# Kernel tuning notes

Measured on AMD Instinct MI355X. Metric: run time of the kernel, lower is better.

## Reference

```python
import jax, jax.numpy as jnp
import numpy as np

L = 5          # num_layers
N = 50000      # nodes
E = 600000     # edges
D = 128        # num_features == hidden_units
G = 256        # graphs in batch
O = 10         # num_outputs
BN_EPS = 1e-5


def setup_inputs() -> dict:
    key = jax.random.key(0)
    ks = jax.random.split(key, 8)
    x = jax.random.normal(ks[0], (N, D), jnp.float32)
    edge_index = jax.random.randint(ks[1], (2, E), 0, N, jnp.int32)
    edge_attr = jax.random.randint(ks[2], (E, 3), 0, 8, jnp.int32)
    batch = jnp.sort(jax.random.randint(ks[3], (N,), 0, G, jnp.int32))
    s = 0.05
    return {
        "x": x,
        "edge_index": edge_index,
        "edge_attr": edge_attr,
        "batch": batch,
        "bond_emb": jax.random.normal(ks[4], (L, 3, 8, D), jnp.float32) * s,
        "conv_w1": jax.random.normal(ks[5], (L, D, D), jnp.float32) * s,
        "conv_b1": jnp.zeros((L, D), jnp.float32),
        "conv_bn_gamma": jnp.ones((L, D), jnp.float32),
        "conv_bn_beta": jnp.zeros((L, D), jnp.float32),
        "conv_bn_mean": jnp.zeros((L, D), jnp.float32),
        "conv_bn_var": jnp.ones((L, D), jnp.float32),
        "conv_w2": jax.random.normal(ks[6], (L, D, D), jnp.float32) * s,
        "conv_b2": jnp.zeros((L, D), jnp.float32),
        "bn_gamma": jnp.ones((L, D), jnp.float32),
        "bn_beta": jnp.zeros((L, D), jnp.float32),
        "bn_mean": jnp.zeros((L, D), jnp.float32),
        "bn_var": jnp.ones((L, D), jnp.float32),
        "fc_w": jax.random.normal(ks[7], (L + 1, D, O), jnp.float32) * s,
        "fc_b": jnp.zeros((L + 1, O), jnp.float32),
    }


def _bn_eval(h, gamma, beta, mean, var):
    return (h - mean) * jax.lax.rsqrt(var + BN_EPS) * gamma + beta


def reference(x, edge_index, edge_attr, batch, bond_emb,
              conv_w1, conv_b1, conv_bn_gamma, conv_bn_beta, conv_bn_mean, conv_bn_var,
              conv_w2, conv_b2, bn_gamma, bn_beta, bn_mean, bn_var, fc_w, fc_b):
    src, dst = edge_index[0], edge_index[1]  # x_j = x[src], aggregate at dst
    feat_ids = jnp.arange(3)
    outs = [x]
    for i in range(L):
        # BondEncoder: sum of per-feature embeddings -> [E, D]
        ea = bond_emb[i][feat_ids, edge_attr].sum(axis=1)
        # GINEConv (eps=0): msg = relu(x_j + edge_attr), scatter-add, nn(x + aggr)
        msg = jax.nn.relu(x[src] + ea)
        aggr = jax.ops.segment_sum(msg, dst, num_segments=N)
        h = x + aggr
        h = h @ conv_w1[i] + conv_b1[i]
        h = jax.nn.relu(_bn_eval(h, conv_bn_gamma[i], conv_bn_beta[i], conv_bn_mean[i], conv_bn_var[i]))
        h = h @ conv_w2[i] + conv_b2[i]
        x = jax.nn.relu(_bn_eval(h, bn_gamma[i], bn_beta[i], bn_mean[i], bn_var[i]))
        outs.append(x)
    # global mean pool per layer output, linear head, sum (dropout = identity in eval)
    counts = jax.ops.segment_sum(jnp.ones((N,), x.dtype), batch, num_segments=G)
    inv = 1.0 / jnp.maximum(counts, 1.0)
    out = jnp.zeros((G, O), x.dtype)
    for i, h in enumerate(outs):
        pooled = jax.ops.segment_sum(h, batch, num_segments=G) * inv[:, None]
        out = out + pooled @ fc_w[i] + fc_b[i]
    return out
```

## Files before the change

kernel.cpp:

```cpp
#include <hip/hip_runtime.h>

#define NN 50000
#define EE 600000
#define DD 128
#define GG 256
#define LL 5
#define OO 10
#define BN_EPS 1e-5f
#define CPAD 515
#define ESTRIDE 40

#define B_SCAT  2344
#define B_COMBO 1288
#define B_WT    160
#define B_CVT   3125
#define B_POOL  2048
#define B_PREP  (B_SCAT + B_COMBO + B_WT + B_CVT + B_POOL)

typedef __attribute__((ext_vector_type(8))) short short8;
typedef __attribute__((ext_vector_type(16))) float float16;

__device__ __forceinline__ unsigned short f2b(float f) {
    unsigned u = __float_as_uint(f);
    unsigned r = u + 0x7FFFu + ((u >> 16) & 1u);
    return (unsigned short)(r >> 16);
}
__device__ __forceinline__ unsigned pk2(float lo, float hi) {
    return (unsigned)f2b(lo) | ((unsigned)f2b(hi) << 16);
}
__device__ __forceinline__ float blo(unsigned u) { return __uint_as_float(u << 16); }
__device__ __forceinline__ float bhi(unsigned u) { return __uint_as_float(u & 0xFFFF0000u); }

__device__ __forceinline__ void acc8(float* acc, uint4 xv, uint4 cv) {
    acc[0] += fmaxf(blo(xv.x) + blo(cv.x), 0.f);
    acc[1] += fmaxf(bhi(xv.x) + bhi(cv.x), 0.f);
    acc[2] += fmaxf(blo(xv.y) + blo(cv.y), 0.f);
    acc[3] += fmaxf(bhi(xv.y) + bhi(cv.y), 0.f);
    acc[4] += fmaxf(blo(xv.z) + blo(cv.z), 0.f);
    acc[5] += fmaxf(bhi(xv.z) + bhi(cv.z), 0.f);
    acc[6] += fmaxf(blo(xv.w) + blo(cv.w), 0.f);
    acc[7] += fmaxf(bhi(xv.w) + bhi(cv.w), 0.f);
}

__launch_bounds__(256)
__global__ void prep(const float* __restrict__ x, const int* __restrict__ ei,
                     const int* __restrict__ eattr, const int* __restrict__ batch,
                     const float* __restrict__ bond,
                     const float* __restrict__ w1, const float* __restrict__ w2,
                     unsigned* __restrict__ xb4, unsigned short* __restrict__ combo,
                     short* __restrict__ wt, int* __restrict__ epos,
                     unsigned* __restrict__ e_info, float* __restrict__ pooled0) {
    const int bid = (int)(((long long)blockIdx.x * 1021) % B_PREP);
    const int t = threadIdx.x;
    if (bid < B_SCAT) {
        int e = bid * 256 + t;
        if (e < EE) {
            int dst = ei[EE + e];
            int slot = atomicAdd(&epos[dst], 1);
            if (slot < ESTRIDE) {
                unsigned cidx = (unsigned)eattr[e * 3 + 0] | ((unsigned)eattr[e * 3 + 1] << 3)
                              | ((unsigned)eattr[e * 3 + 2] << 6);
                e_info[dst * ESTRIDE + slot] = (unsigned)ei[e] | (cidx << 16);
            }
        }
    } else if (bid < B_SCAT + B_COMBO) {
        int e = (bid - B_SCAT) * 256 + t;
        if (e < LL * CPAD * DD) {
            int l = e / (CPAD * DD), rem = e - l * (CPAD * DD);
            int c = rem / DD, d = rem - c * DD;
            float s;
            if (c >= 512) s = -1e30f;
            else {
                const float* b_ = bond + (size_t)l * 3 * 8 * DD;
                s = b_[(c & 7) * DD + d] + b_[(8 + ((c >> 3) & 7)) * DD + d]
                  + b_[(16 + (c >> 6)) * DD + d];
            }
            combo[e] = f2b(s);
        }
    } else if (bid < B_SCAT + B_COMBO + B_WT) {
        __shared__ float tile[32][33];
        int b = bid - B_SCAT - B_COMBO;
        int mat = b >> 4, tl = b & 15;
        int k0 = (tl >> 2) * 32, c0 = (tl & 3) * 32;
        const float* W = (mat < 5) ? (w1 + (size_t)mat * DD * DD)
                                   : (w2 + (size_t)(mat - 5) * DD * DD);
        int j = t & 31, q = t >> 5;
#pragma unroll
        for (int rr = 0; rr < 4; ++rr) {
            int row = q + rr * 8;
            tile[row][j] = W[(size_t)(k0 + row) * DD + c0 + j];
        }
        __syncthreads();
#pragma unroll
        for (int rr = 0; rr < 4; ++rr) {
            int cr = q + rr * 8;
            wt[(size_t)mat * DD * DD + (size_t)(c0 + cr) * DD + k0 + j] = (short)f2b(tile[j][cr]);
        }
    } else if (bid < B_SCAT + B_COMBO + B_WT + B_CVT) {
        int gid = (bid - (B_SCAT + B_COMBO + B_WT)) * 256 + t;
        const float4* xp = (const float4*)(x + (size_t)gid * 8);
        float4 a = xp[0], c4 = xp[1];
        uint4 o;
        o.x = pk2(a.x, a.y); o.y = pk2(a.z, a.w);
        o.z = pk2(c4.x, c4.y); o.w = pk2(c4.z, c4.w);
        ((uint4*)xb4)[gid] = o;
    } else {
        __shared__ float sm[DD];
        int b = bid - (B_SCAT + B_COMBO + B_WT + B_CVT);
        int g = b >> 3, s = b & 7;
        int r0, r1;
        {
            int lo = 0, hi = NN;
            while (lo < hi) { int m = (lo + hi) >> 1; if (batch[m] < g) lo = m + 1; else hi = m; }
            r0 = lo;
            lo = 0; hi = NN;
            while (lo < hi) { int m = (lo + hi) >> 1; if (batch[m] < g + 1) lo = m + 1; else hi = m; }
            r1 = lo;
        }
        int col = t & 127, par = t >> 7;
        float ssum = 0.f;
        for (int r = r0 + s * 2 + par; r < r1; r += 16) ssum += x[(size_t)r * DD + col];
        if (par == 0) sm[col] = ssum;
        __syncthreads();
        if (par == 1) {
            float v = sm[col] + ssum;
            if (v != 0.f) atomicAdd(&pooled0[(size_t)g * DD + col], v);
        }
    }
}

__launch_bounds__(256)
__global__ void aggr_csr(const unsigned short* __restrict__ xin,
                         const int* __restrict__ epos,
                         const unsigned* __restrict__ e_info,
                         const unsigned short* __restrict__ combo,
                         unsigned short* __restrict__ hin) {
    const int q = 12500 / 8, rr_ = 12500 % 8;
    int xcd = blockIdx.x & 7, idx = blockIdx.x >> 3;
    int bid = (xcd < rr_ ? xcd * (q + 1) : rr_ * (q + 1) + (xcd - rr_) * q) + idx;
    int node = bid * 4 + (threadIdx.x >> 6);
    int lane = threadIdx.x & 63;
    if (node >= NN) return;
    const int base = node * ESTRIDE;
    int deg = epos[node]; if (deg > ESTRIDE) deg = ESTRIDE;
    const int eg = lane >> 4;
    const int f  = (lane & 15) * 8;

    unsigned i0 = __builtin_nontemporal_load(e_info + base + eg);
    unsigned i1 = __builtin_nontemporal_load(e_info + base + 4 + eg);
    unsigned i2 = __builtin_nontemporal_load(e_info + base + 8 + eg);
    unsigned i3 = __builtin_nontemporal_load(e_info + base + 12 + eg);

    uint4 xv0 = *(const uint4*)&xin[(size_t)(i0 & 0xFFFFu) * DD + f];
    uint4 cv0 = *(const uint4*)&combo[(size_t)(i0 >> 16) * DD + f];
    uint4 xv1 = *(const uint4*)&xin[(size_t)(i1 & 0xFFFFu) * DD + f];
    uint4 cv1 = *(const uint4*)&combo[(size_t)(i1 >> 16) * DD + f];
    uint4 xv2 = *(const uint4*)&xin[(size_t)(i2 & 0xFFFFu) * DD + f];
    uint4 cv2 = *(const uint4*)&combo[(size_t)(i2 >> 16) * DD + f];
    uint4 xv3 = *(const uint4*)&xin[(size_t)(i3 & 0xFFFFu) * DD + f];
    uint4 cv3 = *(const uint4*)&combo[(size_t)(i3 >> 16) * DD + f];

    float acc[8];
#pragma unroll
    for (int i = 0; i < 8; ++i) acc[i] = 0.f;
    acc8(acc, xv0, cv0);
    acc8(acc, xv1, cv1);
    acc8(acc, xv2, cv2);
    acc8(acc, xv3, cv3);

    if (deg > 16) {
        const int pe = base + ((deg + 7) & ~7);
        for (int p = base + 16; p < pe; p += 8) {
            unsigned j0 = __builtin_nontemporal_load(e_info + p + eg);
            unsigned j1 = __builtin_nontemporal_load(e_info + p + 4 + eg);
            uint4 ax0 = *(const uint4*)&xin[(size_t)(j0 & 0xFFFFu) * DD + f];
            uint4 ac0 = *(const uint4*)&combo[(size_t)(j0 >> 16) * DD + f];
            uint4 ax1 = *(const uint4*)&xin[(size_t)(j1 & 0xFFFFu) * DD + f];
            uint4 ac1 = *(const uint4*)&combo[(size_t)(j1 >> 16) * DD + f];
            acc8(acc, ax0, ac0);
            acc8(acc, ax1, ac1);
        }
    }

#pragma unroll
    for (int i = 0; i < 8; ++i) {
        acc[i] += __shfl_xor(acc[i], 16, 64);
        acc[i] += __shfl_xor(acc[i], 32, 64);
    }
    if (lane < 16) {
        uint4 self = *(const uint4*)&xin[(size_t)node * DD + f];
        uint4 o;
        o.x = pk2(acc[0] + blo(self.x), acc[1] + bhi(self.x));
        o.y = pk2(acc[2] + blo(self.y), acc[3] + bhi(self.y));
        o.z = pk2(acc[4] + blo(self.z), acc[5] + bhi(self.z));
        o.w = pk2(acc[6] + blo(self.w), acc[7] + bhi(self.w));
        *(uint4*)&hin[(size_t)node * DD + f] = o;
    }
}

__launch_bounds__(256)
__global__ void conv_fused(const unsigned short* __restrict__ hin,
                           const short* __restrict__ Wt1, const short* __restrict__ Wt2,
                           const float* __restrict__ b1, const float* __restrict__ g1,
                           const float* __restrict__ be1, const float* __restrict__ m1,
                           const float* __restrict__ v1,
                           const float* __restrict__ b2, const float* __restrict__ g2,
                           const float* __restrict__ be2, const float* __restrict__ m2,
                           const float* __restrict__ v2,
                           const int* __restrict__ batch,
                           unsigned short* __restrict__ outb,
                           float* __restrict__ pool_slot) {
    __shared__ short As[32 * 136];
    __shared__ int sbg[32];
    const int tid  = threadIdx.x;
    const int lane = tid & 63;
    const int wave = tid >> 6;
    const int row0 = blockIdx.x * 32;

    const int col   = wave * 32 + (lane & 31);
    const int khalf = (lane >> 5) * 8;
    const int arow  = lane & 31;
    const int rbase = 4 * (lane >> 5);
    const int gmin  = batch[row0];

    short8 bf[8];
#pragma unroll
    for (int ch = 0; ch < 8; ++ch)
        bf[ch] = *(const short8*)&Wt1[col * DD + ch * 16 + khalf];

    const float sc1 = g1[col] * rsqrtf(v1[col] + BN_EPS);
    const float sh1 = fmaf(b1[col] - m1[col], sc1, be1[col]);
    const float sc2 = g2[col] * rsqrtf(v2[col] + BN_EPS);
    const float sh2 = fmaf(b2[col] - m2[col], sc2, be2[col]);

    if (tid < 32) {
        int row = row0 + tid;
        sbg[tid] = (row < NN) ? batch[row] - gmin : -1;
    }
    for (int i = tid; i < 512; i += 256) {
        int r = i >> 4, c8 = (i & 15) * 8;
        int row = row0 + r;
        uint4 z = make_uint4(0, 0, 0, 0);
        if (row < NN) z = *(const uint4*)&hin[(size_t)row * DD + c8];
        *(uint4*)&As[r * 136 + c8] = z;
    }
    __syncthreads();

    float16 acc0 = {0.f,0.f,0.f,0.f,0.f,0.f,0.f,0.f,0.f,0.f,0.f,0.f,0.f,0.f,0.f,0.f};
#pragma unroll
    for (int ch = 0; ch < 8; ++ch) {
        short8 a0 = *(const short8*)&As[arow * 136 + ch * 16 + khalf];
        acc0 = __builtin_amdgcn_mfma_f32_32x32x16_bf16(a0, bf[ch], acc0, 0, 0, 0);
    }

#pragma unroll
    for (int ch = 0; ch < 8; ++ch)
        bf[ch] = *(const short8*)&Wt2[col * DD + ch * 16 + khalf];

    __syncthreads();
#pragma unroll
    for (int r = 0; r < 16; ++r) {
        int rl = (r & 3) + 8 * (r >> 2) + rbase;
        As[rl * 136 + col] = (short)f2b(fmaxf(fmaf(acc0[r], sc1, sh1), 0.f));
    }
    __syncthreads();

    acc0 = float16{0.f,0.f,0.f,0.f,0.f,0.f,0.f,0.f,0.f,0.f,0.f,0.f,0.f,0.f,0.f,0.f};
#pragma unroll
    for (int ch = 0; ch < 8; ++ch) {
        short8 a0 = *(const short8*)&As[arow * 136 + ch * 16 + khalf];
        acc0 = __builtin_amdgcn_mfma_f32_32x32x16_bf16(a0, bf[ch], acc0, 0, 0, 0);
    }

    float pg0 = 0.f, pg1 = 0.f, pg2 = 0.f, pg3 = 0.f;
#pragma unroll
    for (int r = 0; r < 16; ++r) {
        int rl  = (r & 3) + 8 * (r >> 2) + rbase;
        int row = row0 + rl;
        float v0 = fmaxf(fmaf(acc0[r], sc2, sh2), 0.f);
        if (row < NN) outb[(size_t)row * DD + col] = f2b(v0);
        int ga = sbg[rl];
        pg0 += (ga == 0) ? v0 : 0.f;
        pg1 += (ga == 1) ? v0 : 0.f;
        pg2 += (ga == 2) ? v0 : 0.f;
        pg3 += (ga == 3) ? v0 : 0.f;
    }
    pg0 += __shfl_down(pg0, 32);
    pg1 += __shfl_down(pg1, 32);
    pg2 += __shfl_down(pg2, 32);
    pg3 += __shfl_down(pg3, 32);
    if (lane < 32) {
        if (pg0 != 0.f)                  atomicAdd(&pool_slot[(gmin    ) * DD + col], pg0);
        if (pg1 != 0.f && gmin + 1 < GG) atomicAdd(&pool_slot[(gmin + 1) * DD + col], pg1);
        if (pg2 != 0.f && gmin + 2 < GG) atomicAdd(&pool_slot[(gmin + 2) * DD + col], pg2);
        if (pg3 != 0.f && gmin + 3 < GG) atomicAdd(&pool_slot[(gmin + 3) * DD + col], pg3);
    }
}

__launch_bounds__(64)
__global__ void head(const int* __restrict__ batch, const float* __restrict__ pooled,
                     const float* __restrict__ fcw, const float* __restrict__ fcb,
                     float* __restrict__ out) {
    int g = blockIdx.x, t = threadIdx.x;
    __shared__ float part[LL + 1][OO];
    int r0, r1;
    {
        int lo = 0, hi = NN;
        while (lo < hi) { int m = (lo + hi) >> 1; if (batch[m] < g) lo = m + 1; else hi = m; }
        r0 = lo;
        lo = 0; hi = NN;
        while (lo < hi) { int m = (lo + hi) >> 1; if (batch[m] < g + 1) lo = m + 1; else hi = m; }
        r1 = lo;
    }
    const float invg = 1.0f / fmaxf((float)(r1 - r0), 1.0f);
    if (t < (LL + 1) * OO) {
        int l = t / OO, o2 = t - l * OO;
        const float* p = pooled + ((size_t)l * GG + g) * DD;
        const float* w = fcw + (size_t)l * DD * OO + o2;
        float s = 0.f;
        for (int d2 = 0; d2 < DD; ++d2) s = fmaf(p[d2], w[(size_t)d2 * OO], s);
        part[l][o2] = s;
    }
    __syncthreads();
    if (t < OO) {
        float sp = 0.f, sb2 = 0.f;
#pragma unroll
        for (int l = 0; l < LL + 1; ++l) { sp += part[l][t]; sb2 += fcb[l * OO + t]; }
        out[g * OO + t] = sp * invg + sb2;
    }
}

extern "C" void kernel_launch(void* const* d_in, const int* in_sizes, int n_in,
                              void* d_out, int out_size, void* d_ws, size_t ws_size,
                              hipStream_t stream) {
    const float* x_in    = (const float*)d_in[0];
    const int*   ei      = (const int*)d_in[1];
    const int*   eattr   = (const int*)d_in[2];
    const int*   batch   = (const int*)d_in[3];
    const float* bond    = (const float*)d_in[4];
    const float* conv_w1 = (const float*)d_in[5];
    const float* conv_b1 = (const float*)d_in[6];
    const float* cbg     = (const float*)d_in[7];
    const float* cbb     = (const float*)d_in[8];
    const float* cbm     = (const float*)d_in[9];
    const float* cbv     = (const float*)d_in[10];
    const float* conv_w2 = (const float*)d_in[11];
    const float* conv_b2 = (const float*)d_in[12];
    const float* bg      = (const float*)d_in[13];
    const float* bb      = (const float*)d_in[14];
    const float* bm      = (const float*)d_in[15];
    const float* bv      = (const float*)d_in[16];
    const float* fcw     = (const float*)d_in[17];
    const float* fcb     = (const float*)d_in[18];
    float* out = (float*)d_out;

    char* base = (char*)d_ws;
    size_t o = 0;
    auto carve = [&](size_t bytes) { void* p = base + o; o += (bytes + 15) & ~(size_t)15; return p; };
    unsigned short* xbA    = (unsigned short*)carve((size_t)NN * DD * 2);
    unsigned short* xbB    = (unsigned short*)carve((size_t)NN * DD * 2);
    unsigned short* combo  = (unsigned short*)carve((size_t)LL * CPAD * DD * 2);
    short*          wt     = (short*)carve((size_t)10 * DD * DD * 2);
    const size_t ZBYTES = (size_t)NN * 4 + (size_t)(LL + 1) * GG * DD * 4;
    int*            epos   = (int*)carve(ZBYTES);
    float*          pooled = (float*)((char*)epos + (size_t)NN * 4);
    unsigned*       e_info = (unsigned*)carve((size_t)NN * ESTRIDE * 4);

    hipMemsetAsync(epos, 0, ZBYTES, stream);
    hipMemsetAsync(e_info, 0x02, (size_t)NN * ESTRIDE * 4, stream);

    prep<<<B_PREP, 256, 0, stream>>>(x_in, ei, eattr, batch, bond, conv_w1, conv_w2,
                                     (unsigned*)xbA, combo, wt, epos, e_info, pooled);

    const int conv_blocks = (NN + 31) / 32;
    const int aggr_blocks = (NN + 3) / 4;
    unsigned short* xin  = xbA;
    unsigned short* xout = xbB;
    for (int i = 0; i < LL; ++i) {
        aggr_csr<<<aggr_blocks, 256, 0, stream>>>(
            xin, epos, e_info, combo + (size_t)i * CPAD * DD, xout);
        conv_fused<<<conv_blocks, 256, 0, stream>>>(
            xout, wt + (size_t)i * DD * DD, wt + (size_t)(5 + i) * DD * DD,
            conv_b1 + (size_t)i * DD, cbg + (size_t)i * DD, cbb + (size_t)i * DD,
            cbm + (size_t)i * DD, cbv + (size_t)i * DD,
            conv_b2 + (size_t)i * DD, bg + (size_t)i * DD, bb + (size_t)i * DD,
            bm + (size_t)i * DD, bv + (size_t)i * DD,
            batch, xin, pooled + (size_t)(i + 1) * GG * DD);
    }
    head<<<GG, 64, 0, stream>>>(batch, pooled, fcw, fcb, out);
}
```

Measured before the change: 423.6 us.

## Fuse edge aggregation into per-layer MLP kernel via shared-memory staging

```diff
diff --git a/kernel.cpp b/kernel.cpp
--- a/kernel.cpp
+++ b/kernel.cpp
@@ -130,98 +130,102 @@
 }
 
 __launch_bounds__(256)
-__global__ void aggr_csr(const unsigned short* __restrict__ xin,
-                         const int* __restrict__ epos,
-                         const unsigned* __restrict__ e_info,
-                         const unsigned short* __restrict__ combo,
-                         unsigned short* __restrict__ hin) {
-    const int q = 12500 / 8, rr_ = 12500 % 8;
-    int xcd = blockIdx.x & 7, idx = blockIdx.x >> 3;
-    int bid = (xcd < rr_ ? xcd * (q + 1) : rr_ * (q + 1) + (xcd - rr_) * q) + idx;
-    int node = bid * 4 + (threadIdx.x >> 6);
-    int lane = threadIdx.x & 63;
-    if (node >= NN) return;
-    const int base = node * ESTRIDE;
-    int deg = epos[node]; if (deg > ESTRIDE) deg = ESTRIDE;
-    const int eg = lane >> 4;
-    const int f  = (lane & 15) * 8;
-
-    unsigned i0 = __builtin_nontemporal_load(e_info + base + eg);
-    unsigned i1 = __builtin_nontemporal_load(e_info + base + 4 + eg);
-    unsigned i2 = __builtin_nontemporal_load(e_info + base + 8 + eg);
-    unsigned i3 = __builtin_nontemporal_load(e_info + base + 12 + eg);
-
-    uint4 xv0 = *(const uint4*)&xin[(size_t)(i0 & 0xFFFFu) * DD + f];
-    uint4 cv0 = *(const uint4*)&combo[(size_t)(i0 >> 16) * DD + f];
-    uint4 xv1 = *(const uint4*)&xin[(size_t)(i1 & 0xFFFFu) * DD + f];
-    uint4 cv1 = *(const uint4*)&combo[(size_t)(i1 >> 16) * DD + f];
-    uint4 xv2 = *(const uint4*)&xin[(size_t)(i2 & 0xFFFFu) * DD + f];
-    uint4 cv2 = *(const uint4*)&combo[(size_t)(i2 >> 16) * DD + f];
-    uint4 xv3 = *(const uint4*)&xin[(size_t)(i3 & 0xFFFFu) * DD + f];
-    uint4 cv3 = *(const uint4*)&combo[(size_t)(i3 >> 16) * DD + f];
-
-    float acc[8];
-#pragma unroll
-    for (int i = 0; i < 8; ++i) acc[i] = 0.f;
-    acc8(acc, xv0, cv0);
-    acc8(acc, xv1, cv1);
-    acc8(acc, xv2, cv2);
-    acc8(acc, xv3, cv3);
-
-    if (deg > 16) {
-        const int pe = base + ((deg + 7) & ~7);
-        for (int p = base + 16; p < pe; p += 8) {
-            unsigned j0 = __builtin_nontemporal_load(e_info + p + eg);
-            unsigned j1 = __builtin_nontemporal_load(e_info + p + 4 + eg);
-            uint4 ax0 = *(const uint4*)&xin[(size_t)(j0 & 0xFFFFu) * DD + f];
-            uint4 ac0 = *(const uint4*)&combo[(size_t)(j0 >> 16) * DD + f];
-            uint4 ax1 = *(const uint4*)&xin[(size_t)(j1 & 0xFFFFu) * DD + f];
-            uint4 ac1 = *(const uint4*)&combo[(size_t)(j1 >> 16) * DD + f];
-            acc8(acc, ax0, ac0);
-            acc8(acc, ax1, ac1);
-        }
-    }
-
-#pragma unroll
-    for (int i = 0; i < 8; ++i) {
-        acc[i] += __shfl_xor(acc[i], 16, 64);
-        acc[i] += __shfl_xor(acc[i], 32, 64);
-    }
-    if (lane < 16) {
-        uint4 self = *(const uint4*)&xin[(size_t)node * DD + f];
-        uint4 o;
-        o.x = pk2(acc[0] + blo(self.x), acc[1] + bhi(self.x));
-        o.y = pk2(acc[2] + blo(self.y), acc[3] + bhi(self.y));
-        o.z = pk2(acc[4] + blo(self.z), acc[5] + bhi(self.z));
-        o.w = pk2(acc[6] + blo(self.w), acc[7] + bhi(self.w));
-        *(uint4*)&hin[(size_t)node * DD + f] = o;
-    }
-}
-
-__launch_bounds__(256)
-__global__ void conv_fused(const unsigned short* __restrict__ hin,
-                           const short* __restrict__ Wt1, const short* __restrict__ Wt2,
-                           const float* __restrict__ b1, const float* __restrict__ g1,
-                           const float* __restrict__ be1, const float* __restrict__ m1,
-                           const float* __restrict__ v1,
-                           const float* __restrict__ b2, const float* __restrict__ g2,
-                           const float* __restrict__ be2, const float* __restrict__ m2,
-                           const float* __restrict__ v2,
-                           const int* __restrict__ batch,
-                           unsigned short* __restrict__ outb,
-                           float* __restrict__ pool_slot) {
+__global__ void layer_fused(const unsigned short* __restrict__ xin,
+                            const int* __restrict__ epos,
+                            const unsigned* __restrict__ e_info,
+                            const unsigned short* __restrict__ combo,
+                            const short* __restrict__ Wt1, const short* __restrict__ Wt2,
+                            const float* __restrict__ b1, const float* __restrict__ g1,
+                            const float* __restrict__ be1, const float* __restrict__ m1,
+                            const float* __restrict__ v1,
+                            const float* __restrict__ b2, const float* __restrict__ g2,
+                            const float* __restrict__ be2, const float* __restrict__ m2,
+                            const float* __restrict__ v2,
+                            const int* __restrict__ batch,
+                            unsigned short* __restrict__ xout,
+                            float* __restrict__ pool_slot) {
     __shared__ short As[32 * 136];
     __shared__ int sbg[32];
     const int tid  = threadIdx.x;
     const int lane = tid & 63;
     const int wave = tid >> 6;
     const int row0 = blockIdx.x * 32;
+    const int gmin = batch[row0];
+
+    if (tid < 32) {
+        int row = row0 + tid;
+        sbg[tid] = (row < NN) ? batch[row] - gmin : -1;
+    }
+
+    const int eg = lane >> 4;
+    const int f  = (lane & 15) * 8;
+    for (int k = 0; k < 8; ++k) {
+        const int nl = wave * 8 + k;
+        const int node = row0 + nl;
+        if (node < NN) {
+            const int base = node * ESTRIDE;
+            unsigned i0 = __builtin_nontemporal_load(e_info + base + eg);
+            unsigned i1 = __builtin_nontemporal_load(e_info + base + 4 + eg);
+            unsigned i2 = __builtin_nontemporal_load(e_info + base + 8 + eg);
+            unsigned i3 = __builtin_nontemporal_load(e_info + base + 12 + eg);
+
+            uint4 xv0 = *(const uint4*)&xin[(size_t)(i0 & 0xFFFFu) * DD + f];
+            uint4 cv0 = *(const uint4*)&combo[(size_t)(i0 >> 16) * DD + f];
+            uint4 xv1 = *(const uint4*)&xin[(size_t)(i1 & 0xFFFFu) * DD + f];
+            uint4 cv1 = *(const uint4*)&combo[(size_t)(i1 >> 16) * DD + f];
+            uint4 xv2 = *(const uint4*)&xin[(size_t)(i2 & 0xFFFFu) * DD + f];
+            uint4 cv2 = *(const uint4*)&combo[(size_t)(i2 >> 16) * DD + f];
+            uint4 xv3 = *(const uint4*)&xin[(size_t)(i3 & 0xFFFFu) * DD + f];
+            uint4 cv3 = *(const uint4*)&combo[(size_t)(i3 >> 16) * DD + f];
+
+            float acc[8];
+#pragma unroll
+            for (int i = 0; i < 8; ++i) acc[i] = 0.f;
+            acc8(acc, xv0, cv0);
+            acc8(acc, xv1, cv1);
+            acc8(acc, xv2, cv2);
+            acc8(acc, xv3, cv3);
+
+            int deg = epos[node];
+            if (deg > 16) {
+                if (deg > ESTRIDE) deg = ESTRIDE;
+                const int pe = base + ((deg + 7) & ~7);
+                for (int p = base + 16; p < pe; p += 8) {
+                    unsigned j0 = __builtin_nontemporal_load(e_info + p + eg);
+                    unsigned j1 = __builtin_nontemporal_load(e_info + p + 4 + eg);
+                    uint4 ax0 = *(const uint4*)&xin[(size_t)(j0 & 0xFFFFu) * DD + f];
+                    uint4 ac0 = *(const uint4*)&combo[(size_t)(j0 >> 16) * DD + f];
+                    uint4 ax1 = *(const uint4*)&xin[(size_t)(j1 & 0xFFFFu) * DD + f];
+                    uint4 ac1 = *(const uint4*)&combo[(size_t)(j1 >> 16) * DD + f];
+                    acc8(acc, ax0, ac0);
+                    acc8(acc, ax1, ac1);
+                }
+            }
+
+#pragma unroll
+            for (int i = 0; i < 8; ++i) {
+                acc[i] += __shfl_xor(acc[i], 16, 64);
+                acc[i] += __shfl_xor(acc[i], 32, 64);
+            }
+            if (lane < 16) {
+                uint4 self = *(const uint4*)&xin[(size_t)node * DD + f];
+                uint4 o;
+                o.x = pk2(acc[0] + blo(self.x), acc[1] + bhi(self.x));
+                o.y = pk2(acc[2] + blo(self.y), acc[3] + bhi(self.y));
+                o.z = pk2(acc[4] + blo(self.z), acc[5] + bhi(self.z));
+                o.w = pk2(acc[6] + blo(self.w), acc[7] + bhi(self.w));
+                *(uint4*)&As[nl * 136 + f] = o;
+            }
+        } else if (lane < 16) {
+            *(uint4*)&As[nl * 136 + f] = make_uint4(0, 0, 0, 0);
+        }
+    }
+    __syncthreads();
 
     const int col   = wave * 32 + (lane & 31);
     const int khalf = (lane >> 5) * 8;
     const int arow  = lane & 31;
     const int rbase = 4 * (lane >> 5);
-    const int gmin  = batch[row0];
 
     short8 bf[8];
 #pragma unroll
@@ -233,19 +237,6 @@
     const float sc2 = g2[col] * rsqrtf(v2[col] + BN_EPS);
     const float sh2 = fmaf(b2[col] - m2[col], sc2, be2[col]);
 
-    if (tid < 32) {
-        int row = row0 + tid;
-        sbg[tid] = (row < NN) ? batch[row] - gmin : -1;
-    }
-    for (int i = tid; i < 512; i += 256) {
-        int r = i >> 4, c8 = (i & 15) * 8;
-        int row = row0 + r;
-        uint4 z = make_uint4(0, 0, 0, 0);
-        if (row < NN) z = *(const uint4*)&hin[(size_t)row * DD + c8];
-        *(uint4*)&As[r * 136 + c8] = z;
-    }
-    __syncthreads();
-
     float16 acc0 = {0.f,0.f,0.f,0.f,0.f,0.f,0.f,0.f,0.f,0.f,0.f,0.f,0.f,0.f,0.f,0.f};
 #pragma unroll
     for (int ch = 0; ch < 8; ++ch) {
@@ -278,7 +269,7 @@
         int rl  = (r & 3) + 8 * (r >> 2) + rbase;
         int row = row0 + rl;
         float v0 = fmaxf(fmaf(acc0[r], sc2, sh2), 0.f);
-        if (row < NN) outb[(size_t)row * DD + col] = f2b(v0);
+        if (row < NN) xout[(size_t)row * DD + col] = f2b(v0);
         int ga = sbg[rl];
         pg0 += (ga == 0) ? v0 : 0.f;
         pg1 += (ga == 1) ? v0 : 0.f;
@@ -372,20 +363,19 @@
     prep<<<B_PREP, 256, 0, stream>>>(x_in, ei, eattr, batch, bond, conv_w1, conv_w2,
                                      (unsigned*)xbA, combo, wt, epos, e_info, pooled);
 
-    const int conv_blocks = (NN + 31) / 32;
-    const int aggr_blocks = (NN + 3) / 4;
-    unsigned short* xin  = xbA;
-    unsigned short* xout = xbB;
+    const int layer_blocks = (NN + 31) / 32;
+    unsigned short* xcur = xbA;
+    unsigned short* xnxt = xbB;
     for (int i = 0; i < LL; ++i) {
-        aggr_csr<<<aggr_blocks, 256, 0, stream>>>(
-            xin, epos, e_info, combo + (size_t)i * CPAD * DD, xout);
-        conv_fused<<<conv_blocks, 256, 0, stream>>>(
-            xout, wt + (size_t)i * DD * DD, wt + (size_t)(5 + i) * DD * DD,
+        layer_fused<<<layer_blocks, 256, 0, stream>>>(
+            xcur, epos, e_info, combo + (size_t)i * CPAD * DD,
+            wt + (size_t)i * DD * DD, wt + (size_t)(5 + i) * DD * DD,
             conv_b1 + (size_t)i * DD, cbg + (size_t)i * DD, cbb + (size_t)i * DD,
             cbm + (size_t)i * DD, cbv + (size_t)i * DD,
             conv_b2 + (size_t)i * DD, bg + (size_t)i * DD, bb + (size_t)i * DD,
             bm + (size_t)i * DD, bv + (size_t)i * DD,
-            batch, xin, pooled + (size_t)(i + 1) * GG * DD);
+            batch, xnxt, pooled + (size_t)(i + 1) * GG * DD);
+        unsigned short* tmp = xcur; xcur = xnxt; xnxt = tmp;
     }
     head<<<GG, 64, 0, stream>>>(batch, pooled, fcw, fcb, out);
 }
```

Measured after the change: 429.8 us. No clear change (+1.5%).
